# Kernel optimization log

Measured on AMD Instinct MI355X. Metric: run time of the kernel, lower is better.

## Reference

```python
import jax, jax.numpy as jnp
import numpy as np

# 4 fixed corner index matrices from the original corner() helper
_IDX = np.array([[[-1., 0.], [0., -1.]],
                 [[-1., 0.], [0.,  1.]],
                 [[ 1., 0.], [0.,  1.]],
                 [[ 1., 0.], [0., -1.]]], dtype=np.float32)  # (4,2,2)


def _bounds(h, Corner, ac, bd):
    """lower/upper bound clamps for h of shape (2,1,B); returns (lb, ub) each (2,1,B)."""
    relu = jax.nn.relu
    hx = h[0, 0, :]  # (B,)
    hy = h[1, 0, :]
    # lower_bound_x
    c = jnp.where(bd >= 0, Corner[0, 1], Corner[1, 1])
    g = -relu((hy - c) * bd) + jnp.abs(Corner[1, 0] - Corner[0, 0])
    lbx = -relu(g) + jnp.where(bd >= 0, Corner[1, 0], Corner[0, 0])
    # upper_bound_x
    c = jnp.where(bd >= 0, Corner[3, 1], Corner[2, 1])
    g = -relu((hy - c) * bd) + jnp.abs(Corner[2, 0] - Corner[3, 0])
    ubx = -relu(g) + jnp.where(bd >= 0, Corner[2, 0], Corner[3, 0])
    # lower_bound_y
    c = jnp.where(ac >= 0, Corner[0, 0], Corner[3, 0])
    g = -relu((hx - c) * ac) + jnp.abs(Corner[0, 1] - Corner[3, 1])
    lby = -relu(g) + jnp.where(ac >= 0, Corner[3, 1], Corner[0, 1])
    # upper_bound_y
    c = jnp.where(ac >= 0, Corner[1, 0], Corner[2, 0])
    g = -relu((hx - c) * ac) + jnp.abs(Corner[1, 1] - Corner[2, 1])
    uby = -relu(g) + jnp.where(ac >= 0, Corner[2, 1], Corner[1, 1])
    lb = jnp.stack((lbx, lby))[:, None, :]  # (2,1,B)
    ub = jnp.stack((ubx, uby))[:, None, :]
    return lb, ub


def _forward(x_seq, target, returns, w_input, w_hidden, b_hidden, w_fc1, w_fc2, w_rotate):
    D, T, B = x_seq.shape  # D = dim_size = 2
    idx = jnp.asarray(_IDX, dtype=x_seq.dtype)
    # Corner: (4,2)
    Corner = (w_rotate @ (idx @ b_hidden).T).T + target
    ac = w_rotate[1, 0] / w_rotate[0, 0]
    bd = w_rotate[0, 1] / w_rotate[1, 1]
    Wi = w_input.reshape(D, 1, 1)
    Wh = w_hidden.reshape(D, 1, 1)
    W1 = w_fc1.reshape(D, 1, 1)
    W2 = w_fc2.reshape(D, 1, 1)

    def recur(x, h):
        lb, ub = _bounds(h, Corner, ac, bd)
        g1 = jax.nn.relu(Wi * x + Wh * h - lb)
        g2 = jax.nn.relu(W1 * g1 + ub - lb)
        return W2 * g2 + ub

    h0 = x_seq[:, 0, :][:, None, :]                              # (2,1,B)
    xs = jnp.moveaxis(x_seq[:, 1:, :], 1, 0)[:, :, None, :]      # (T-1,2,1,B)
    rs = jnp.moveaxis(returns[:, : T - 1, :], 1, 0)[:, :, None, :]

    def step(h, xr):
        x, r = xr
        adj = h * (1 + r) / (1 + jnp.sum(h * r, axis=0, keepdims=True))
        hn = recur(x, adj)
        return hn, hn

    hT, outs = jax.lax.scan(step, h0, (xs, rs))                  # outs: (T-1,2,1,B)
    output = jnp.concatenate([h0, jnp.moveaxis(outs[:, :, 0, :], 0, 1)], axis=1)  # (2,T,B)
    return output, hT


def setup_inputs() -> dict:
    key = jax.random.key(0)
    ks = jax.random.split(key, 9)
    D, T, B = 2, 512, 16384
    inp = jax.random.normal(ks[0], (D, T, B), dtype=jnp.float32)
    target = jax.random.normal(ks[1], (D,), dtype=jnp.float32)
    # small positive per-step returns so the 512-step recurrence is well conditioned
    returns_partition = jax.random.uniform(ks[2], (D, T, B), dtype=jnp.float32) * 0.01
    hidden = jnp.zeros((D, 1, B), dtype=jnp.float32)  # overwritten at t=0, kept for signature fidelity
    s = 0.3  # weight scale keeps |W2*W1*Wh| < 1 -> stable recurrence
    w_input = jax.random.normal(ks[3], (D, 1), dtype=jnp.float32) * s
    w_hidden = jax.random.normal(ks[4], (D, 1), dtype=jnp.float32) * s
    b_hidden = jax.random.normal(ks[5], (D,), dtype=jnp.float32) * s
    w_fc1 = jax.random.normal(ks[6], (D, 1), dtype=jnp.float32) * s
    w_fc2 = jax.random.normal(ks[7], (D, 1), dtype=jnp.float32) * s
    w_rotate = jnp.eye(D, dtype=jnp.float32) + jax.random.normal(ks[8], (D, D), dtype=jnp.float32) * s
    return {"input": inp, "target": target, "returns_partition": returns_partition,
            "hidden": hidden, "w_input": w_input, "w_hidden": w_hidden,
            "b_hidden": b_hidden, "w_fc1": w_fc1, "w_fc2": w_fc2, "w_rotate": w_rotate}


def reference(input, target, returns_partition, hidden, w_input, w_hidden,
              b_hidden, w_fc1, w_fc2, w_rotate):
    return _forward(input, target, returns_partition, w_input, w_hidden,
                    b_hidden, w_fc1, w_fc2, w_rotate)
```

## Files before the change

### kernel.cpp

```cpp
#include <hip/hip_runtime.h>


#define U 8

__global__ __launch_bounds__(64, 1)
void ntr_rnn_kernel(const float* __restrict__ xin,
                    const float* __restrict__ target,
                    const float* __restrict__ rets,
                    const float* __restrict__ w_input,
                    const float* __restrict__ w_hidden,
                    const float* __restrict__ b_hidden,
                    const float* __restrict__ w_fc1,
                    const float* __restrict__ w_fc2,
                    const float* __restrict__ w_rotate,
                    float* __restrict__ out,
                    int T, int B)
{
    const int b = blockIdx.x * blockDim.x + threadIdx.x;
    if (b >= B) return;

    const float r00 = w_rotate[0], r01 = w_rotate[1];
    const float r10 = w_rotate[2], r11 = w_rotate[3];
    const float bh0 = b_hidden[0], bh1 = b_hidden[1];
    const float t0  = target[0],   t1  = target[1];

    const float vx[4] = {-bh0, -bh0, bh0, bh0};
    const float vy[4] = {-bh1,  bh1, bh1, -bh1};
    float C[4][2];
#pragma unroll
    for (int c = 0; c < 4; ++c) {
        C[c][0] = r00 * vx[c] + r01 * vy[c] + t0;
        C[c][1] = r10 * vx[c] + r11 * vy[c] + t1;
    }
    const float ac = r10 / r00;
    const float bd = r01 / r11;
    const bool bdp = (bd >= 0.0f);
    const bool acp = (ac >= 0.0f);

    const float cbd_l    = (bdp ? C[0][1] : C[1][1]) * bd;
    const float k_lbx    = fabsf(C[1][0] - C[0][0]);
    const float base_lbx = bdp ? C[1][0] : C[0][0];

    const float cbd_u    = (bdp ? C[3][1] : C[2][1]) * bd;
    const float k_ubx    = fabsf(C[2][0] - C[3][0]);
    const float base_ubx = bdp ? C[2][0] : C[3][0];

    const float cac_l    = (acp ? C[0][0] : C[3][0]) * ac;
    const float k_lby    = fabsf(C[0][1] - C[3][1]);
    const float base_lby = acp ? C[3][1] : C[0][1];

    const float cac_u    = (acp ? C[1][0] : C[2][0]) * ac;
    const float k_uby    = fabsf(C[1][1] - C[2][1]);
    const float base_uby = acp ? C[2][1] : C[1][1];

    const float Wi0 = w_input[0],  Wi1 = w_input[1];
    const float Wh0 = w_hidden[0], Wh1 = w_hidden[1];
    const float W10 = w_fc1[0],    W11 = w_fc1[1];
    const float W20 = w_fc2[0],    W21 = w_fc2[1];

    const size_t TB = (size_t)T * B;
    const float* px0 = xin  + b;
    const float* px1 = xin  + TB + b;
    const float* pr0 = rets + b;
    const float* pr1 = rets + TB + b;
    float* po0 = out + b;
    float* po1 = out + TB + b;

    float hx = px0[0];
    float hy = px1[0];
    __builtin_nontemporal_store(hx, po0);
    __builtin_nontemporal_store(hy, po1);

    auto step = [&](float x0, float x1, float r0, float r1, int t) {
        float denom = fmaf(hx, r0, fmaf(hy, r1, 1.0f));
        float inv   = __builtin_amdgcn_rcpf(denom);
        float nx    = fmaf(hx, r0, hx);
        float ny    = fmaf(hy, r1, hy);
        float adjx  = nx * inv;
        float adjy  = ny * inv;
        float lbx = base_lbx - fmaxf(k_lbx - fmaxf(fmaf(adjy, bd, -cbd_l), 0.0f), 0.0f);
        float ubx = base_ubx - fmaxf(k_ubx - fmaxf(fmaf(adjy, bd, -cbd_u), 0.0f), 0.0f);
        float lby = base_lby - fmaxf(k_lby - fmaxf(fmaf(adjx, ac, -cac_l), 0.0f), 0.0f);
        float uby = base_uby - fmaxf(k_uby - fmaxf(fmaf(adjx, ac, -cac_u), 0.0f), 0.0f);
        float pre0 = Wi0 * x0;
        float pre1 = Wi1 * x1;
        float g1x = fmaxf(fmaf(Wh0, adjx, pre0) - lbx, 0.0f);
        float g1y = fmaxf(fmaf(Wh1, adjy, pre1) - lby, 0.0f);
        float g2x = fmaxf(fmaf(W10, g1x, ubx - lbx), 0.0f);
        float g2y = fmaxf(fmaf(W11, g1y, uby - lby), 0.0f);
        hx = fmaf(W20, g2x, ubx);
        hy = fmaf(W21, g2y, uby);
        __builtin_nontemporal_store(hx, po0 + (size_t)t * B);
        __builtin_nontemporal_store(hy, po1 + (size_t)t * B);
    };

#define LOADG(gx0, gx1, gr0, gr1, tb)                         \
    {                                                         \
        _Pragma("unroll")                                     \
        for (int i = 0; i < U; ++i) {                         \
            gx0[i] = px0[(size_t)((tb) + i) * B];             \
            gx1[i] = px1[(size_t)((tb) + i) * B];             \
            gr0[i] = pr0[(size_t)((tb) + i - 1) * B];         \
            gr1[i] = pr1[(size_t)((tb) + i - 1) * B];         \
        }                                                     \
    }

#define COMPUTEG(gx0, gx1, gr0, gr1, tb)                      \
    {                                                         \
        _Pragma("unroll")                                     \
        for (int i = 0; i < U; ++i)                           \
            step(gx0[i], gx1[i], gr0[i], gr1[i], (tb) + i);   \
    }

    if (T == 512) {
        float Ax0[U], Ax1[U], Ar0[U], Ar1[U];
        float Bx0[U], Bx1[U], Br0[U], Br1[U];
        float Cx0[U], Cx1[U], Cr0[U], Cr1[U];

        float Px0[7], Px1[7], Pr0[7], Pr1[7];
#pragma unroll
        for (int i = 0; i < 7; ++i) {
            int t = 1 + i;
            Px0[i] = px0[(size_t)t * B];
            Px1[i] = px1[(size_t)t * B];
            Pr0[i] = pr0[(size_t)(t - 1) * B];
            Pr1[i] = pr1[(size_t)(t - 1) * B];
        }
        LOADG(Ax0, Ax1, Ar0, Ar1, 8);

#pragma unroll
        for (int i = 0; i < 7; ++i)
            step(Px0[i], Px1[i], Pr0[i], Pr1[i], 1 + i);

        LOADG(Bx0, Bx1, Br0, Br1, 16);

        int tc = 8;
        for (int r = 0; r < 20; ++r) {
            LOADG(Cx0, Cx1, Cr0, Cr1, tc + 16);
            COMPUTEG(Ax0, Ax1, Ar0, Ar1, tc);  tc += 8;
            LOADG(Ax0, Ax1, Ar0, Ar1, tc + 16);
            COMPUTEG(Bx0, Bx1, Br0, Br1, tc);  tc += 8;
            LOADG(Bx0, Bx1, Br0, Br1, tc + 16);
            COMPUTEG(Cx0, Cx1, Cr0, Cr1, tc);  tc += 8;
        }
        LOADG(Cx0, Cx1, Cr0, Cr1, 504);
        COMPUTEG(Ax0, Ax1, Ar0, Ar1, 488);
        COMPUTEG(Bx0, Bx1, Br0, Br1, 496);
        COMPUTEG(Cx0, Cx1, Cr0, Cr1, 504);
    } else {
        for (int t = 1; t < T; ++t) {
            float x0 = px0[(size_t)t * B];
            float x1 = px1[(size_t)t * B];
            float r0 = pr0[(size_t)(t - 1) * B];
            float r1 = pr1[(size_t)(t - 1) * B];
            step(x0, x1, r0, r1, t);
        }
    }

    __builtin_nontemporal_store(hx, out + 2 * TB + b);
    __builtin_nontemporal_store(hy, out + 2 * TB + B + b);
}

extern "C" void kernel_launch(void* const* d_in, const int* in_sizes, int n_in,
                              void* d_out, int out_size, void* d_ws, size_t ws_size,
                              hipStream_t stream) {
    const float* xin      = (const float*)d_in[0];
    const float* target   = (const float*)d_in[1];
    const float* rets     = (const float*)d_in[2];
    const float* w_input  = (const float*)d_in[4];
    const float* w_hidden = (const float*)d_in[5];
    const float* b_hidden = (const float*)d_in[6];
    const float* w_fc1    = (const float*)d_in[7];
    const float* w_fc2    = (const float*)d_in[8];
    const float* w_rotate = (const float*)d_in[9];
    float* out = (float*)d_out;

    const int B = in_sizes[3] / 2;
    const int T = in_sizes[0] / in_sizes[3];

    const int threads = 64;
    const int blocks  = (B + threads - 1) / threads;
    hipLaunchKernelGGL(ntr_rnn_kernel, dim3(blocks), dim3(threads), 0, stream,
                       xin, target, rets, w_input, w_hidden, b_hidden,
                       w_fc1, w_fc2, w_rotate, out, T, B);
}
```

Measured before the change: 198.4 us.

## Restructure prefetch ring to four 4-step slots with pointer-bumped addressing

```diff
diff --git a/kernel.cpp b/kernel.cpp
--- a/kernel.cpp
+++ b/kernel.cpp
@@ -1,7 +1,5 @@
 #include <hip/hip_runtime.h>
 
-
-#define U 8
 
 __global__ __launch_bounds__(64, 1)
 void ntr_rnn_kernel(const float* __restrict__ xin,
@@ -59,19 +57,19 @@
     const float W20 = w_fc2[0],    W21 = w_fc2[1];
 
     const size_t TB = (size_t)T * B;
-    const float* px0 = xin  + b;
-    const float* px1 = xin  + TB + b;
-    const float* pr0 = rets + b;
-    const float* pr1 = rets + TB + b;
-    float* po0 = out + b;
-    float* po1 = out + TB + b;
+    const float* gx0 = xin;
+    const float* gx1 = xin + TB;
+    const float* gr0 = rets;
+    const float* gr1 = rets + TB;
+    float* o0 = out;
+    float* o1 = out + TB;
 
-    float hx = px0[0];
-    float hy = px1[0];
-    __builtin_nontemporal_store(hx, po0);
-    __builtin_nontemporal_store(hy, po1);
+    float hx = gx0[b];
+    float hy = gx1[b];
+    __builtin_nontemporal_store(hx, &o0[b]);
+    __builtin_nontemporal_store(hy, &o1[b]);
 
-    auto step = [&](float x0, float x1, float r0, float r1, int t) {
+    auto step = [&](float x0, float x1, float r0, float r1) {
         float denom = fmaf(hx, r0, fmaf(hy, r1, 1.0f));
         float inv   = __builtin_amdgcn_rcpf(denom);
         float nx    = fmaf(hx, r0, hx);
@@ -90,70 +88,83 @@
         float g2y = fmaxf(fmaf(W11, g1y, uby - lby), 0.0f);
         hx = fmaf(W20, g2x, ubx);
         hy = fmaf(W21, g2y, uby);
-        __builtin_nontemporal_store(hx, po0 + (size_t)t * B);
-        __builtin_nontemporal_store(hy, po1 + (size_t)t * B);
     };
 
-#define LOADG(gx0, gx1, gr0, gr1, tb)                         \
-    {                                                         \
-        _Pragma("unroll")                                     \
-        for (int i = 0; i < U; ++i) {                         \
-            gx0[i] = px0[(size_t)((tb) + i) * B];             \
-            gx1[i] = px1[(size_t)((tb) + i) * B];             \
-            gr0[i] = pr0[(size_t)((tb) + i - 1) * B];         \
-            gr1[i] = pr1[(size_t)((tb) + i - 1) * B];         \
-        }                                                     \
-    }
+    if (T == 512) {
+        struct Slot { float x0[4], x1[4], r0[4], r1[4]; };
+        Slot S0, S1, S2, S3;
 
-#define COMPUTEG(gx0, gx1, gr0, gr1, tb)                      \
-    {                                                         \
-        _Pragma("unroll")                                     \
-        for (int i = 0; i < U; ++i)                           \
-            step(gx0[i], gx1[i], gr0[i], gr1[i], (tb) + i);   \
-    }
+        const size_t B4 = 4 * (size_t)B;
 
-    if (T == 512) {
-        float Ax0[U], Ax1[U], Ar0[U], Ar1[U];
-        float Bx0[U], Bx1[U], Br0[U], Br1[U];
-        float Cx0[U], Cx1[U], Cr0[U], Cr1[U];
+        const float* lx0 = gx0 + B4;
+        const float* lx1 = gx1 + B4;
+        const float* lr0 = gr0 + 3 * (size_t)B;
+        const float* lr1 = gr1 + 3 * (size_t)B;
+        float* so0 = o0 + B4;
+        float* so1 = o1 + B4;
 
-        float Px0[7], Px1[7], Pr0[7], Pr1[7];
+#define LOADS(S)                                              \
+        do {                                                  \
+            _Pragma("unroll")                                 \
+            for (int i = 0; i < 4; ++i) {                     \
+                S.x0[i] = lx0[i * B + b];                     \
+                S.x1[i] = lx1[i * B + b];                     \
+                S.r0[i] = lr0[i * B + b];                     \
+                S.r1[i] = lr1[i * B + b];                     \
+            }                                                 \
+            lx0 += B4; lx1 += B4; lr0 += B4; lr1 += B4;       \
+        } while (0)
+
+#define COMPS(S)                                              \
+        do {                                                  \
+            _Pragma("unroll")                                 \
+            for (int i = 0; i < 4; ++i) {                     \
+                step(S.x0[i], S.x1[i], S.r0[i], S.r1[i]);     \
+                __builtin_nontemporal_store(hx, &so0[i * B + b]); \
+                __builtin_nontemporal_store(hy, &so1[i * B + b]); \
+            }                                                 \
+            so0 += B4; so1 += B4;                             \
+        } while (0)
+
+        float Px0[3], Px1[3], Pr0[3], Pr1[3];
 #pragma unroll
-        for (int i = 0; i < 7; ++i) {
-            int t = 1 + i;
-            Px0[i] = px0[(size_t)t * B];
-            Px1[i] = px1[(size_t)t * B];
-            Pr0[i] = pr0[(size_t)(t - 1) * B];
-            Pr1[i] = pr1[(size_t)(t - 1) * B];
+        for (int i = 0; i < 3; ++i) {
+            Px0[i] = gx0[(1 + i) * B + b];
+            Px1[i] = gx1[(1 + i) * B + b];
+            Pr0[i] = gr0[i * B + b];
+            Pr1[i] = gr1[i * B + b];
         }
-        LOADG(Ax0, Ax1, Ar0, Ar1, 8);
+        LOADS(S0);
+        LOADS(S1);
+        LOADS(S2);
 
 #pragma unroll
-        for (int i = 0; i < 7; ++i)
-            step(Px0[i], Px1[i], Pr0[i], Pr1[i], 1 + i);
+        for (int i = 0; i < 3; ++i) {
+            step(Px0[i], Px1[i], Pr0[i], Pr1[i]);
+            __builtin_nontemporal_store(hx, &o0[(1 + i) * B + b]);
+            __builtin_nontemporal_store(hy, &o1[(1 + i) * B + b]);
+        }
 
-        LOADG(Bx0, Bx1, Br0, Br1, 16);
-
-        int tc = 8;
-        for (int r = 0; r < 20; ++r) {
-            LOADG(Cx0, Cx1, Cr0, Cr1, tc + 16);
-            COMPUTEG(Ax0, Ax1, Ar0, Ar1, tc);  tc += 8;
-            LOADG(Ax0, Ax1, Ar0, Ar1, tc + 16);
-            COMPUTEG(Bx0, Bx1, Br0, Br1, tc);  tc += 8;
-            LOADG(Bx0, Bx1, Br0, Br1, tc + 16);
-            COMPUTEG(Cx0, Cx1, Cr0, Cr1, tc);  tc += 8;
+        for (int r = 0; r < 31; ++r) {
+            LOADS(S3);  COMPS(S0);
+            LOADS(S0);  COMPS(S1);
+            LOADS(S1);  COMPS(S2);
+            LOADS(S2);  COMPS(S3);
         }
-        LOADG(Cx0, Cx1, Cr0, Cr1, 504);
-        COMPUTEG(Ax0, Ax1, Ar0, Ar1, 488);
-        COMPUTEG(Bx0, Bx1, Br0, Br1, 496);
-        COMPUTEG(Cx0, Cx1, Cr0, Cr1, 504);
+        COMPS(S0);
+        COMPS(S1);
+        COMPS(S2);
+#undef LOADS
+#undef COMPS
     } else {
         for (int t = 1; t < T; ++t) {
-            float x0 = px0[(size_t)t * B];
-            float x1 = px1[(size_t)t * B];
-            float r0 = pr0[(size_t)(t - 1) * B];
-            float r1 = pr1[(size_t)(t - 1) * B];
-            step(x0, x1, r0, r1, t);
+            float x0 = gx0[(size_t)t * B + b];
+            float x1 = gx1[(size_t)t * B + b];
+            float r0 = gr0[(size_t)(t - 1) * B + b];
+            float r1 = gr1[(size_t)(t - 1) * B + b];
+            step(x0, x1, r0, r1);
+            __builtin_nontemporal_store(hx, &o0[(size_t)t * B + b]);
+            __builtin_nontemporal_store(hy, &o1[(size_t)t * B + b]);
         }
     }
 
```

After: 206.7 us. +4.2%, slower.
